# Kernel optimization log

Measured on AMD Instinct MI355X. Metric: run time of the kernel, lower is better.

## Reference

```python
import jax, jax.numpy as jnp
import numpy as np

B, L, H, N, COND = 32, 32768, 32, 16, 4
N2 = N // 2  # S4D stores N/2 complex conjugate-pair modes


def setup_inputs() -> dict:
    key = jax.random.key(0)
    ks = jax.random.split(key, 8)
    x = jax.random.normal(ks[0], (B, L, H), jnp.float32)
    cond = jax.random.normal(ks[1], (B, COND), jnp.float32)
    # S4D kernel parameters (state-spaces minimal S4D init)
    log_dt = np.log(1e-3) + jax.random.uniform(ks[2], (H,), jnp.float32) * (np.log(1e-1) - np.log(1e-3))
    C_re = jax.random.normal(ks[3], (H, N2), jnp.float32) * (0.5 ** 0.5)
    C_im = jax.random.normal(ks[4], (H, N2), jnp.float32) * (0.5 ** 0.5)
    log_A_real = jnp.log(0.5 * jnp.ones((H, N2), jnp.float32))
    A_imag = jnp.pi * jnp.tile(jnp.arange(N2, dtype=jnp.float32), (H, 1))
    D = jax.random.normal(ks[5], (H,), jnp.float32)
    # FiLM linear: cond -> (gamma, beta)
    film_W = jax.random.normal(ks[6], (COND, 2 * H), jnp.float32) / np.sqrt(COND)
    film_b = jnp.zeros((2 * H,), jnp.float32)
    return dict(x=x, cond=cond, log_dt=log_dt, C_re=C_re, C_im=C_im,
                log_A_real=log_A_real, A_imag=A_imag, D=D,
                film_W=film_W, film_b=film_b)


def reference(x, cond, log_dt, C_re, C_im, log_A_real, A_imag, D, film_W, film_b):
    # x: (B, L, H) -> DSSM over channel-major layout (B, H, L)
    u = jnp.transpose(x, (0, 2, 1))  # B H L
    # --- S4D kernel: K[h, l] = 2 * Re( sum_n C~_hn * exp(dt_h * A_hn * l) )
    dt = jnp.exp(log_dt)[:, None]                      # (H, 1)
    A = -jnp.exp(log_A_real) + 1j * A_imag             # (H, N2) complex
    dtA = A * dt                                       # (H, N2)
    Ct = (C_re + 1j * C_im) * (jnp.exp(dtA) - 1.0) / A # discretized C
    vand = jnp.exp(dtA[:, :, None] * jnp.arange(L, dtype=jnp.float32))  # (H, N2, L)
    K = 2.0 * jnp.einsum('hn,hnl->hl', Ct, vand).real  # (H, L)
    # --- causal convolution via FFT on length-2L circular pad
    n_fft = 2 * L
    y = jnp.fft.irfft(jnp.fft.rfft(u, n=n_fft) * jnp.fft.rfft(K, n=n_fft), n=n_fft)[..., :L]
    y = y + u * D[:, None]                             # skip connection
    y = jnp.transpose(y, (0, 2, 1))                    # back to (B, L, H)
    # --- FiLM conditioning
    gb = cond @ film_W + film_b                        # (B, 2H)
    gamma, beta = gb[:, :H], gb[:, H:]
    y = gamma[:, None, :] * y + beta[:, None, :]
    # --- activation
    return jax.nn.gelu(y)
```

## Files before the change

### kernel.cpp

```cpp
#include <hip/hip_runtime.h>

#define BB 32
#define LL 32768
#define HH 32
#define NN2 8
#define NCOND 4
#define NCHUNK 128
#define LC (LL / NCHUNK)

#define PARAM_OFF 0
#define WLC_OFF   1024
#define FILM_OFF  1536
#define S_OFF     4096
#define SZ_S      (BB * HH * NCHUNK * NN2 * 2)
#define ZIN_OFF   (S_OFF + SZ_S)

__global__ void setup_kernel(const float* __restrict__ log_dt,
                             const float* __restrict__ C_re,
                             const float* __restrict__ C_im,
                             const float* __restrict__ log_A_real,
                             const float* __restrict__ A_imag,
                             const float* __restrict__ cond,
                             const float* __restrict__ film_W,
                             const float* __restrict__ film_b,
                             float* __restrict__ ws) {
  int idx = blockIdx.x * blockDim.x + threadIdx.x;
  if (idx < HH * NN2) {
    int h = idx >> 3;
    float dt = expf(log_dt[h]);
    float ar = -expf(log_A_real[idx]);
    float ai = A_imag[idx];
    float dr = ar * dt, di = ai * dt;
    float er = expf(dr);
    float wr = er * cosf(di);
    float wi = er * sinf(di);
    float den = ar * ar + ai * ai;
    float tr = ((wr - 1.f) * ar + wi * ai) / den;
    float ti = (wi * ar - (wr - 1.f) * ai) / den;
    float cr = C_re[idx], ci = C_im[idx];
    float ctr = 2.f * (cr * tr - ci * ti);
    float cti = 2.f * (cr * ti + ci * tr);
    float* p = ws + PARAM_OFF + idx * 4;
    p[0] = wr; p[1] = wi; p[2] = ctr; p[3] = cti;
    float eL  = expf(dr * (float)LC);
    float wlr = eL * cosf(di * (float)LC);
    float wli = eL * sinf(di * (float)LC);
    float* q = ws + WLC_OFF + idx * 2;
    q[0] = wlr; q[1] = wli;
  }
  int f = idx - HH * NN2;
  if (f >= 0 && f < BB * HH) {
    int b = f >> 5, h = f & (HH - 1);
    float g  = film_b[h];
    float be = film_b[h + HH];
    #pragma unroll
    for (int c2 = 0; c2 < NCOND; c2++) {
      float cv = cond[b * NCOND + c2];
      g  = fmaf(cv, film_W[c2 * 2 * HH + h], g);
      be = fmaf(cv, film_W[c2 * 2 * HH + HH + h], be);
    }
    float* p = ws + FILM_OFF + f * 2;
    p[0] = g; p[1] = be;
  }
}

__global__ __launch_bounds__(256) void pass_a(const float* __restrict__ x,
                                              float* __restrict__ ws) {
  const int flat = blockIdx.x * 256 + threadIdx.x;
  const int h = flat & (HH - 1);
  const int c = (flat >> 5) & (NCHUNK - 1);
  const int b = flat >> 12;
  const float4* pp = (const float4*)(ws + PARAM_OFF);
  float wr[NN2], wi[NN2], zr[NN2], zi[NN2];
  #pragma unroll
  for (int n = 0; n < NN2; n++) {
    float4 p = pp[h * NN2 + n];
    wr[n] = p.x; wi[n] = p.y;
    zr[n] = 0.f; zi[n] = 0.f;
  }
  const float* xp = x + ((size_t)b * LL + (size_t)c * LC) * HH + h;
  for (int i = 0; i < LC; i += 8) {
    float u[8];
    #pragma unroll
    for (int j = 0; j < 8; j++) u[j] = xp[(size_t)(i + j) * HH];
    #pragma unroll
    for (int j = 0; j < 8; j++) {
      #pragma unroll
      for (int n = 0; n < NN2; n++) {
        float t0  = fmaf(-wi[n], zi[n], u[j]);
        float nzr = fmaf(wr[n], zr[n], t0);
        float nzi = fmaf(wr[n], zi[n], wi[n] * zr[n]);
        zr[n] = nzr; zi[n] = nzi;
      }
    }
  }
  float4* Sp = (float4*)(ws + S_OFF) + (size_t)flat * 4;
  #pragma unroll
  for (int q = 0; q < 4; q++)
    Sp[q] = make_float4(zr[q * 2], zi[q * 2], zr[q * 2 + 1], zi[q * 2 + 1]);
}

__global__ void pass_b(float* __restrict__ ws) {
  int idx = blockIdx.x * blockDim.x + threadIdx.x;
  int n = idx & (NN2 - 1);
  int h = (idx >> 3) & (HH - 1);
  int b = idx >> 8;
  float wlr = ws[WLC_OFF + (h * NN2 + n) * 2];
  float wli = ws[WLC_OFF + (h * NN2 + n) * 2 + 1];
  float Zr = 0.f, Zi = 0.f;
  const size_t stride = (size_t)HH * NN2 * 2;
  size_t base = ((size_t)b * NCHUNK * HH + h) * (NN2 * 2) + n * 2;
  for (int c = 0; c < NCHUNK; c++) {
    size_t e = base + (size_t)c * stride;
    ws[ZIN_OFF + e]     = Zr;
    ws[ZIN_OFF + e + 1] = Zi;
    float sr = ws[S_OFF + e];
    float si = ws[S_OFF + e + 1];
    float nZr = fmaf(wlr, Zr, fmaf(-wli, Zi, sr));
    float nZi = fmaf(wlr, Zi, fmaf(wli, Zr, si));
    Zr = nZr; Zi = nZi;
  }
}

__global__ __launch_bounds__(256) void pass_c(const float* __restrict__ x,
                                              const float* __restrict__ Dv,
                                              float* __restrict__ out,
                                              float* __restrict__ ws) {
  const int flat = blockIdx.x * 256 + threadIdx.x;
  const int h = flat & (HH - 1);
  const int c = (flat >> 5) & (NCHUNK - 1);
  const int b = flat >> 12;
  float wr[NN2], wi[NN2], ctr[NN2], cti[NN2], zr[NN2], zi[NN2];
  const float4* pp = (const float4*)(ws + PARAM_OFF);
  #pragma unroll
  for (int n = 0; n < NN2; n++) {
    float4 p = pp[h * NN2 + n];
    wr[n] = p.x; wi[n] = p.y; ctr[n] = p.z; cti[n] = p.w;
  }
  const float4* Zp = (const float4*)(ws + ZIN_OFF) + (size_t)flat * 4;
  #pragma unroll
  for (int q = 0; q < 4; q++) {
    float4 z = Zp[q];
    zr[q * 2] = z.x; zi[q * 2] = z.y; zr[q * 2 + 1] = z.z; zi[q * 2 + 1] = z.w;
  }
  float gamma = ws[FILM_OFF + ((size_t)b * HH + h) * 2];
  float beta  = ws[FILM_OFF + ((size_t)b * HH + h) * 2 + 1];
  float dcoef = Dv[h];
  const size_t off = ((size_t)b * LL + (size_t)c * LC) * HH + h;
  const float* xp = x + off;
  float* op = out + off;
  for (int i = 0; i < LC; i += 8) {
    float u[8];
    #pragma unroll
    for (int j = 0; j < 8; j++) u[j] = xp[(size_t)(i + j) * HH];
    #pragma unroll
    for (int j = 0; j < 8; j++) {
      float acc = 0.f;
      #pragma unroll
      for (int n = 0; n < NN2; n++) {
        float t0  = fmaf(-wi[n], zi[n], u[j]);
        float nzr = fmaf(wr[n], zr[n], t0);
        float nzi = fmaf(wr[n], zi[n], wi[n] * zr[n]);
        zr[n] = nzr; zi[n] = nzi;
        acc = fmaf(ctr[n], nzr, acc);
        acc = fmaf(-cti[n], nzi, acc);
      }
      float y = fmaf(dcoef, u[j], acc);
      y = fmaf(gamma, y, beta);
      float y3   = y * y * y;
      float targ = 0.7978845608f * fmaf(0.044715f, y3, y);
      float e    = __expf(2.f * targ);
      float th   = 1.f - __fdividef(2.f, e + 1.f);
      op[(size_t)(i + j) * HH] = 0.5f * y * (1.f + th);
    }
  }
}

extern "C" void kernel_launch(void* const* d_in, const int* in_sizes, int n_in,
                              void* d_out, int out_size, void* d_ws, size_t ws_size,
                              hipStream_t stream) {
  const float* x          = (const float*)d_in[0];
  const float* cond       = (const float*)d_in[1];
  const float* log_dt     = (const float*)d_in[2];
  const float* C_re       = (const float*)d_in[3];
  const float* C_im       = (const float*)d_in[4];
  const float* log_A_real = (const float*)d_in[5];
  const float* A_imag     = (const float*)d_in[6];
  const float* Dv         = (const float*)d_in[7];
  const float* film_W     = (const float*)d_in[8];
  const float* film_b     = (const float*)d_in[9];
  float* out = (float*)d_out;
  float* ws  = (float*)d_ws;

  setup_kernel<<<5, 256, 0, stream>>>(log_dt, C_re, C_im, log_A_real, A_imag,
                                      cond, film_W, film_b, ws);
  pass_a<<<(BB * HH * NCHUNK) / 256, 256, 0, stream>>>(x, ws);
  pass_b<<<(BB * HH * NN2) / 256, 256, 0, stream>>>(ws);
  pass_c<<<(BB * HH * NCHUNK) / 256, 256, 0, stream>>>(x, Dv, out, ws);
}
```

Measured before the change: 315.5 us.

## Pack complex recurrences into v2f packed FMAs and double the chunk count

Rewrites the per-mode complex recurrence in pass_a and pass_c to use two-wide float vectors, so the compiler can emit packed FMA instructions (v_pk_fma_f32) that handle two modes per instruction. Chunks per sequence go from 128 to 256, doubling thread-level parallelism for the scan passes. Parameters and chunk states are re-laid out as separate real and imaginary planes, and pass_b now updates the state buffer in place instead of writing a separate Zin array. The trade-off is a longer sequential loop in pass_b, a two-lane accumulator that is reduced at the end, and a changed summation order.

New measurement: 313.8 us. No clear change (-0.5%).

```diff
diff --git a/kernel.cpp b/kernel.cpp
--- a/kernel.cpp
+++ b/kernel.cpp
@@ -1,19 +1,24 @@
 #include <hip/hip_runtime.h>
+
+typedef float v2f __attribute__((ext_vector_type(2)));
 
 #define BB 32
 #define LL 32768
 #define HH 32
 #define NN2 8
 #define NCOND 4
-#define NCHUNK 128
+#define NCHUNK 256
 #define LC (LL / NCHUNK)
 
 #define PARAM_OFF 0
 #define WLC_OFF   1024
 #define FILM_OFF  1536
 #define S_OFF     4096
-#define SZ_S      (BB * HH * NCHUNK * NN2 * 2)
-#define ZIN_OFF   (S_OFF + SZ_S)
+#define SZ_S      (BB * HH * NCHUNK * 16)
+
+static __device__ __forceinline__ v2f vfma(v2f a, v2f b, v2f c) {
+  return __builtin_elementwise_fma(a, b, c);
+}
 
 __global__ void setup_kernel(const float* __restrict__ log_dt,
                              const float* __restrict__ C_re,
@@ -26,7 +31,7 @@
                              float* __restrict__ ws) {
   int idx = blockIdx.x * blockDim.x + threadIdx.x;
   if (idx < HH * NN2) {
-    int h = idx >> 3;
+    int h = idx >> 3, n = idx & (NN2 - 1);
     float dt = expf(log_dt[h]);
     float ar = -expf(log_A_real[idx]);
     float ai = A_imag[idx];
@@ -40,8 +45,8 @@
     float cr = C_re[idx], ci = C_im[idx];
     float ctr = 2.f * (cr * tr - ci * ti);
     float cti = 2.f * (cr * ti + ci * tr);
-    float* p = ws + PARAM_OFF + idx * 4;
-    p[0] = wr; p[1] = wi; p[2] = ctr; p[3] = cti;
+    float* p = ws + PARAM_OFF + h * 32;
+    p[n] = wr; p[n + 8] = wi; p[n + 16] = ctr; p[n + 24] = cti;
     float eL  = expf(dr * (float)LC);
     float wlr = eL * cosf(di * (float)LC);
     float wli = eL * sinf(di * (float)LC);
@@ -69,14 +74,13 @@
   const int flat = blockIdx.x * 256 + threadIdx.x;
   const int h = flat & (HH - 1);
   const int c = (flat >> 5) & (NCHUNK - 1);
-  const int b = flat >> 12;
-  const float4* pp = (const float4*)(ws + PARAM_OFF);
-  float wr[NN2], wi[NN2], zr[NN2], zi[NN2];
-  #pragma unroll
-  for (int n = 0; n < NN2; n++) {
-    float4 p = pp[h * NN2 + n];
-    wr[n] = p.x; wi[n] = p.y;
-    zr[n] = 0.f; zi[n] = 0.f;
+  const int b = flat >> 13;
+  const v2f* pp = (const v2f*)(ws + PARAM_OFF + h * 32);
+  v2f wr[4], wi[4], zr[4], zi[4];
+  #pragma unroll
+  for (int g = 0; g < 4; g++) {
+    wr[g] = pp[g]; wi[g] = pp[4 + g];
+    zr[g] = (v2f){0.f, 0.f}; zi[g] = (v2f){0.f, 0.f};
   }
   const float* xp = x + ((size_t)b * LL + (size_t)c * LC) * HH + h;
   for (int i = 0; i < LC; i += 8) {
@@ -85,19 +89,19 @@
     for (int j = 0; j < 8; j++) u[j] = xp[(size_t)(i + j) * HH];
     #pragma unroll
     for (int j = 0; j < 8; j++) {
+      v2f us = (v2f){u[j], u[j]};
       #pragma unroll
-      for (int n = 0; n < NN2; n++) {
-        float t0  = fmaf(-wi[n], zi[n], u[j]);
-        float nzr = fmaf(wr[n], zr[n], t0);
-        float nzi = fmaf(wr[n], zi[n], wi[n] * zr[n]);
-        zr[n] = nzr; zi[n] = nzi;
+      for (int g = 0; g < 4; g++) {
+        v2f t0  = vfma(-wi[g], zi[g], us);
+        v2f nzr = vfma(wr[g], zr[g], t0);
+        v2f nzi = vfma(wr[g], zi[g], wi[g] * zr[g]);
+        zr[g] = nzr; zi[g] = nzi;
       }
     }
   }
-  float4* Sp = (float4*)(ws + S_OFF) + (size_t)flat * 4;
-  #pragma unroll
-  for (int q = 0; q < 4; q++)
-    Sp[q] = make_float4(zr[q * 2], zi[q * 2], zr[q * 2 + 1], zi[q * 2 + 1]);
+  v2f* Sp = (v2f*)(ws + S_OFF + (size_t)flat * 16);
+  #pragma unroll
+  for (int g = 0; g < 4; g++) { Sp[g] = zr[g]; Sp[4 + g] = zi[g]; }
 }
 
 __global__ void pass_b(float* __restrict__ ws) {
@@ -108,14 +112,14 @@
   float wlr = ws[WLC_OFF + (h * NN2 + n) * 2];
   float wli = ws[WLC_OFF + (h * NN2 + n) * 2 + 1];
   float Zr = 0.f, Zi = 0.f;
-  const size_t stride = (size_t)HH * NN2 * 2;
-  size_t base = ((size_t)b * NCHUNK * HH + h) * (NN2 * 2) + n * 2;
+  const size_t stride = (size_t)HH * 16;
+  size_t base = ((size_t)b * NCHUNK * HH + h) * 16 + n;
   for (int c = 0; c < NCHUNK; c++) {
-    size_t e = base + (size_t)c * stride;
-    ws[ZIN_OFF + e]     = Zr;
-    ws[ZIN_OFF + e + 1] = Zi;
-    float sr = ws[S_OFF + e];
-    float si = ws[S_OFF + e + 1];
+    float* pr = ws + S_OFF + base + (size_t)c * stride;
+    float sr = pr[0];
+    float si = pr[8];
+    pr[0] = Zr;
+    pr[8] = Zi;
     float nZr = fmaf(wlr, Zr, fmaf(-wli, Zi, sr));
     float nZi = fmaf(wlr, Zi, fmaf(wli, Zr, si));
     Zr = nZr; Zi = nZi;
@@ -129,20 +133,16 @@
   const int flat = blockIdx.x * 256 + threadIdx.x;
   const int h = flat & (HH - 1);
   const int c = (flat >> 5) & (NCHUNK - 1);
-  const int b = flat >> 12;
-  float wr[NN2], wi[NN2], ctr[NN2], cti[NN2], zr[NN2], zi[NN2];
-  const float4* pp = (const float4*)(ws + PARAM_OFF);
-  #pragma unroll
-  for (int n = 0; n < NN2; n++) {
-    float4 p = pp[h * NN2 + n];
-    wr[n] = p.x; wi[n] = p.y; ctr[n] = p.z; cti[n] = p.w;
-  }
-  const float4* Zp = (const float4*)(ws + ZIN_OFF) + (size_t)flat * 4;
-  #pragma unroll
-  for (int q = 0; q < 4; q++) {
-    float4 z = Zp[q];
-    zr[q * 2] = z.x; zi[q * 2] = z.y; zr[q * 2 + 1] = z.z; zi[q * 2 + 1] = z.w;
-  }
+  const int b = flat >> 13;
+  const v2f* pp = (const v2f*)(ws + PARAM_OFF + h * 32);
+  v2f wr[4], wi[4], ctr[4], cti[4], zr[4], zi[4];
+  #pragma unroll
+  for (int g = 0; g < 4; g++) {
+    wr[g] = pp[g]; wi[g] = pp[4 + g]; ctr[g] = pp[8 + g]; cti[g] = pp[12 + g];
+  }
+  const v2f* Zp = (const v2f*)(ws + S_OFF + (size_t)flat * 16);
+  #pragma unroll
+  for (int g = 0; g < 4; g++) { zr[g] = Zp[g]; zi[g] = Zp[4 + g]; }
   float gamma = ws[FILM_OFF + ((size_t)b * HH + h) * 2];
   float beta  = ws[FILM_OFF + ((size_t)b * HH + h) * 2 + 1];
   float dcoef = Dv[h];
@@ -155,17 +155,19 @@
     for (int j = 0; j < 8; j++) u[j] = xp[(size_t)(i + j) * HH];
     #pragma unroll
     for (int j = 0; j < 8; j++) {
-      float acc = 0.f;
+      v2f us = (v2f){u[j], u[j]};
+      v2f acc = (v2f){0.f, 0.f};
       #pragma unroll
-      for (int n = 0; n < NN2; n++) {
-        float t0  = fmaf(-wi[n], zi[n], u[j]);
-        float nzr = fmaf(wr[n], zr[n], t0);
-        float nzi = fmaf(wr[n], zi[n], wi[n] * zr[n]);
-        zr[n] = nzr; zi[n] = nzi;
-        acc = fmaf(ctr[n], nzr, acc);
-        acc = fmaf(-cti[n], nzi, acc);
+      for (int g = 0; g < 4; g++) {
+        v2f t0  = vfma(-wi[g], zi[g], us);
+        v2f nzr = vfma(wr[g], zr[g], t0);
+        v2f nzi = vfma(wr[g], zi[g], wi[g] * zr[g]);
+        zr[g] = nzr; zi[g] = nzi;
+        acc = vfma(ctr[g], nzr, acc);
+        acc = vfma(-cti[g], nzi, acc);
       }
-      float y = fmaf(dcoef, u[j], acc);
+      float y = acc.x + acc.y;
+      y = fmaf(dcoef, u[j], y);
       y = fmaf(gamma, y, beta);
       float y3   = y * y * y;
       float targ = 0.7978845608f * fmaf(0.044715f, y3, y);
```
